# Kernel optimization log

Hardware: AMD Instinct MI355X
Metric: run time of the kernel (lower is better)

The kernel has to match this reference:

```python
import jax, jax.numpy as jnp
import numpy as np

B, NT, NP = 4096, 2048, 1024
DT = 1e-3


def _cum_trap(y, dx):
    # cumulative trapezoid along last dim, zero-prepended (preserve_dims=True)
    c = jnp.cumsum((y[..., 1:] + y[..., :-1]) * (0.5 * dx), axis=-1)
    return jnp.concatenate([jnp.zeros_like(y[..., :1]), c], axis=-1)


def _trapz(y, dx):
    return jnp.sum(y[..., :-1] + y[..., 1:], axis=-1) * (0.5 * dx)


def _renorm(f, dx):
    # square-normalize so each trace integrates to 1 (valid pdf)
    sq = f * f
    return sq / _trapz(sq, dx)[..., None]


def _natural_cubic_coeffs(p, q):
    # p: [NP] uniform knots, q: [B, NP] values -> per-interval coeffs a,b,c,d [B, NP-1]
    h = p[1] - p[0]
    n = p.shape[0]
    rhs = 6.0 * (q[..., :-2] - 2.0 * q[..., 1:-1] + q[..., 2:]) / (h * h)  # [B, n-2]
    m = n - 2
    A = 4.0 * jnp.eye(m, dtype=q.dtype) + jnp.eye(m, k=1, dtype=q.dtype) + jnp.eye(m, k=-1, dtype=q.dtype)
    M_int = jnp.linalg.solve(A, rhs.T).T                      # [B, n-2]
    zero = jnp.zeros_like(q[..., :1])
    M = jnp.concatenate([zero, M_int, zero], axis=-1)          # natural BC: M0 = Mn = 0
    a = q[..., :-1]
    b = (q[..., 1:] - q[..., :-1]) / h - h * (2.0 * M[..., :-1] + M[..., 1:]) / 6.0
    c = M[..., :-1] / 2.0
    d = (M[..., 1:] - M[..., :-1]) / (6.0 * h)
    return a, b, c, d


def _spline_eval(p, coeffs, x):
    # evaluate batched natural cubic splines at x: [B, NT]
    a, b, c, d = coeffs
    idx = jnp.clip(jnp.searchsorted(p, x, side='right') - 1, 0, p.shape[0] - 2)  # [B, NT]
    s = x - p[idx]
    ag = jnp.take_along_axis(a, idx, axis=-1)
    bg = jnp.take_along_axis(b, idx, axis=-1)
    cg = jnp.take_along_axis(c, idx, axis=-1)
    dg = jnp.take_along_axis(d, idx, axis=-1)
    return ag + s * (bg + s * (cg + s * dg))


def setup_inputs() -> dict:
    key = jax.random.key(0)
    k1, k2 = jax.random.split(key)
    f = jax.random.normal(k1, (B, NT), dtype=jnp.float32)
    obs_data = jax.random.normal(k2, (B, NT), dtype=jnp.float32)
    t = jnp.arange(NT, dtype=jnp.float32) * DT
    p = jnp.linspace(0.0, 1.0, NP, dtype=jnp.float32)
    return {"f": f, "obs_data": obs_data, "t": t, "p": p}


def reference(f, obs_data, t, p):
    dt = t[1] - t[0]
    # ---- __init__: build per-trace quantile splines from obs_data ----
    obs_tilde = _renorm(obs_data, dt)                 # [B, NT] pdf
    cdf_obs = _cum_trap(obs_tilde, dt)                # [B, NT] cdf
    # true_quantile: step lookup q(p) = t[searchsorted(cdf, p)]
    idx = jax.vmap(lambda c: jnp.searchsorted(c, p))(cdf_obs)
    idx = jnp.clip(idx, 0, t.shape[0] - 1)
    q = t[idx]                                        # [B, NP]
    coeffs = _natural_cubic_coeffs(p, q)
    # ---- forward: W2 distance ----
    f_tilde = _renorm(f, dt)                          # [B, NT]
    F = _cum_trap(f_tilde, dt)                        # [B, NT] cdf of f
    off_diag = _spline_eval(p, coeffs, F)             # Q_obs(F(t)) [B, NT]
    diff = (t[None, :] - off_diag) ** 2
    integrated = _trapz(diff * f_tilde, dt)           # [B]
    return integrated.sum()
```

## Files before the change

### kernel.cpp

```cpp
#include <hip/hip_runtime.h>

#define NBATCH 4096
#define NT 2048
#define NP 1024
#define NTH 256
#define EPT 8
#define MSZ 1022
#define KT 4
#define IMGW 14

__device__ __forceinline__ int pQ(int x) { return x + (x >> 3) + 9; }
__device__ __forceinline__ int pM(int x) { return x + (x >> 3); }

__global__ __launch_bounds__(NTH, 2) void w2loss_kernel(
    const float* __restrict__ f,
    const float* __restrict__ obs,
    float* __restrict__ partial)
{
    __shared__ float sQp[1168];
    __shared__ float sMp[1152];
    __shared__ float sH[NTH];
    __shared__ float sPow[IMGW];
    __shared__ float sWSA[4], sWSB[4];
    __shared__ float sSqA[2], sSqB[2];
    __shared__ float sRed[4];

    const int tid  = threadIdx.x;
    const int lane = tid & 63;
    const int wid  = tid >> 6;
    const int b    = blockIdx.x;
    const int base = tid * EPT;

    const float dt      = 0.001f;
    const float half_dt = 0.0005f;
    const float h       = 0.00097751710654936461f;
    const float inv_h   = 1023.0f;
    const float inv_h2  = 1046529.0f;
    const float h6      = h * (1.0f / 6.0f);
    const float ih6     = inv_h * (1.0f / 6.0f);

    const float* orow = obs + (size_t)b * NT;
    const float* frow = f   + (size_t)b * NT;
    float4 o0 = *reinterpret_cast<const float4*>(orow + base);
    float4 o1 = *reinterpret_cast<const float4*>(orow + base + 4);
    float4 g0 = *reinterpret_cast<const float4*>(frow + base);
    float4 g1 = *reinterpret_cast<const float4*>(frow + base + 4);

    if (tid < IMGW) {
        const float rho = -0.26794919243112270f;
        float v = 1.0f;
        for (int i = 0; i < tid; ++i) v *= rho;
        sPow[tid] = v;
    }

    float prefA[EPT], prefB[EPT];
    {
        float s0;
        s0 = o0.x*o0.x; prefA[0] = s0;
        s0 = o0.y*o0.y; prefA[1] = prefA[0] + s0;
        s0 = o0.z*o0.z; prefA[2] = prefA[1] + s0;
        s0 = o0.w*o0.w; prefA[3] = prefA[2] + s0;
        s0 = o1.x*o1.x; prefA[4] = prefA[3] + s0;
        s0 = o1.y*o1.y; prefA[5] = prefA[4] + s0;
        s0 = o1.z*o1.z; prefA[6] = prefA[5] + s0;
        s0 = o1.w*o1.w; prefA[7] = prefA[6] + s0;
        s0 = g0.x*g0.x; prefB[0] = s0;
        s0 = g0.y*g0.y; prefB[1] = prefB[0] + s0;
        s0 = g0.z*g0.z; prefB[2] = prefB[1] + s0;
        s0 = g0.w*g0.w; prefB[3] = prefB[2] + s0;
        s0 = g1.x*g1.x; prefB[4] = prefB[3] + s0;
        s0 = g1.y*g1.y; prefB[5] = prefB[4] + s0;
        s0 = g1.z*g1.z; prefB[6] = prefB[5] + s0;
        s0 = g1.w*g1.w; prefB[7] = prefB[6] + s0;
    }
    float sqA7 = o1.w * o1.w;
    float sqB7 = g1.w * g1.w;
    sH[tid] = sqA7;

    float tsA = prefA[EPT - 1], tsB = prefB[EPT - 1];
    float wsA = tsA, wsB = tsB;
#pragma unroll
    for (int off = 1; off < 64; off <<= 1) {
        float uA = __shfl_up(wsA, off);
        float uB = __shfl_up(wsB, off);
        if (lane >= off) { wsA += uA; wsB += uB; }
    }
    if (lane == 63) { sWSA[wid] = wsA; sWSB[wid] = wsB; }
    if (tid == 0)       { sSqA[0] = prefA[0]; sSqB[0] = prefB[0]; }
    if (tid == NTH - 1) { sSqA[1] = sqA7;     sSqB[1] = sqB7; }
    __syncthreads();

    float exclA = wsA - tsA, exclB = wsB - tsB;
    if (wid > 0) { exclA += sWSA[0]; exclB += sWSB[0]; }
    if (wid > 1) { exclA += sWSA[1]; exclB += sWSB[1]; }
    if (wid > 2) { exclA += sWSA[2]; exclB += sWSB[2]; }
    float totA = sWSA[0] + sWSA[1] + sWSA[2] + sWSA[3];
    float totB = sWSB[0] + sWSB[1] + sWSB[2] + sWSB[3];
    float sq0A = sSqA[0], sq0B = sSqB[0];
    float invSA = 1.0f / (half_dt * (2.0f * totA - sSqA[1] - sq0A));
    float invSB = 1.0f / (half_dt * (2.0f * totB - sSqB[1] - sq0B));

    {
        float cm;
        if (tid == 0) cm = -1.0f;
        else {
            float sqprev = sH[tid - 1];
            cm = half_dt * (((exclA - sqprev) + exclA) - sq0A) * invSA;
        }
        float Pm = exclA;
#pragma unroll
        for (int e = 0; e < EPT; ++e) {
            int j = base + e;
            float Pj = exclA + prefA[e];
            float cc = (j == 0) ? 0.0f : half_dt * (Pm + Pj - sq0A) * invSA;
            int kLo = (int)floorf(cm * inv_h) + 1;
            int kHi = (int)floorf(cc * inv_h);
            if (kLo < 0) kLo = 0;
            if (j == NT - 1) kHi = NP - 1;
            else {
                if (e == EPT - 1) kHi += 1;
                if (kHi > NP - 1) kHi = NP - 1;
            }
            float qv = (float)j * dt;
            for (int k = kLo; k <= kHi; ++k) sQp[pQ(k)] = qv;
            cm = cc;
            Pm = Pj;
        }
    }
    __syncthreads();

    {
        const float Cg = 0.28867513459481288f;
        const float CP[KT + 1] = {
            1.0f, -0.26794919243112270f, 0.071796769724490830f,
            -0.019237886466840586f, 0.0051547761428899979f };
        const int k0 = tid * 4;

        float qw[14];
#pragma unroll
        for (int x = 0; x < 14; ++x) qw[x] = sQp[pQ(k0 - 5 + x)];

        float r[12];
#pragma unroll
        for (int x = 0; x < 12; ++x) {
            int gi = k0 - 5 + x;
            float v = 6.0f * (qw[x] - 2.0f * qw[x + 1] + qw[x + 2]) * inv_h2;
            r[x] = (gi >= 0 && gi < MSZ) ? v : 0.0f;
        }

        float T1 = 0.0f, T2 = 0.0f;
        if (tid < 4) {
            float qe[15];
#pragma unroll
            for (int x = 0; x < 15; ++x) qe[x] = sQp[pQ(x)];
#pragma unroll
            for (int x = 0; x < IMGW - 1; ++x) {
                float rr = 6.0f * (qe[x] - 2.0f * qe[x + 1] + qe[x + 2]) * inv_h2;
                T1 += sPow[x + 1] * rr;
            }
        }
        if (tid >= NTH - 4) {
            float qe[15];
#pragma unroll
            for (int x = 0; x < 15; ++x) qe[x] = sQp[pQ(1009 + x)];
#pragma unroll
            for (int x = 0; x < IMGW - 1; ++x) {
                float rr = 6.0f * (qe[x] - 2.0f * qe[x + 1] + qe[x + 2]) * inv_h2;
                T2 += sPow[13 - x] * rr;
            }
        }

#pragma unroll
        for (int e = 0; e < 4; ++e) {
            int k = k0 + e;
            float acc = 0.0f;
#pragma unroll
            for (int d = -KT; d <= KT; ++d) {
                int ad = d < 0 ? -d : d;
                acc += CP[ad] * r[e + 4 + d];
            }
            if (k < IMGW)        acc -= sPow[k] * T1;
            if (1023 - k < IMGW) acc -= sPow[1023 - k] * T2;
            float mv = Cg * acc;
            if (k == 0 || k == NP - 1) mv = 0.0f;
            sMp[pM(k)] = mv;
        }
    }
    __syncthreads();

    float local = 0.0f;
    float term0 = 0.0f, term7 = 0.0f;
    {
        const float c1B = half_dt * invSB;
        const float K0  = (2.0f * exclB - sq0B) * c1B;
        float tj = (float)base * dt;
#pragma unroll
        for (int e = 0; e < EPT; ++e) {
            float Gj = (e ? prefB[e - 1] : 0.0f) + prefB[e];
            float Fj = __builtin_fmaf(Gj, c1B, K0);
            float sqe = e ? (prefB[e] - prefB[e - 1]) : prefB[0];
            float kf = Fj * inv_h;
            kf = fminf(fmaxf(kf, 0.0f), 1022.0f);
            int k = (int)kf;
            float s = __builtin_fmaf(-h, (float)k, Fj);
            float q0 = sQp[pQ(k)];
            float q1 = sQp[pQ(k + 1)];
            float M0 = sMp[pM(k)];
            float M1 = sMp[pM(k + 1)];
            float bco = (q1 - q0) * inv_h - (2.0f * M0 + M1) * h6;
            float od  = q0 + s * (bco + s * (0.5f * M0 + s * (M1 - M0) * ih6));
            float dd  = tj - od;
            float term = dd * dd * sqe;
            local += term;
            if (e == 0) term0 = term;
            if (e == EPT - 1) term7 = term;
            tj += dt;
        }
    }
    if (tid == 0)       local -= 0.5f * term0;
    if (tid == NTH - 1) local -= 0.5f * term7;

#pragma unroll
    for (int off = 32; off > 0; off >>= 1) local += __shfl_down(local, off);
    if (lane == 0) sRed[wid] = local;
    __syncthreads();
    if (tid == 0) partial[b] = (sRed[0] + sRed[1] + sRed[2] + sRed[3]) * (dt * invSB);
}

__global__ __launch_bounds__(NTH) void w2loss_reduce(
    const float* __restrict__ partial, float* __restrict__ out)
{
    __shared__ float sRed[4];
    const int tid  = threadIdx.x;
    const int lane = tid & 63;
    const int wid  = tid >> 6;
    float s = 0.0f;
#pragma unroll
    for (int i = 0; i < 16; i += 4) {
        float4 v = *reinterpret_cast<const float4*>(partial + tid * 16 + i);
        s += v.x + v.y + v.z + v.w;
    }
#pragma unroll
    for (int off = 32; off > 0; off >>= 1) s += __shfl_down(s, off);
    if (lane == 0) sRed[wid] = s;
    __syncthreads();
    if (tid == 0) out[0] = sRed[0] + sRed[1] + sRed[2] + sRed[3];
}

extern "C" void kernel_launch(void* const* d_in, const int* in_sizes, int n_in,
                              void* d_out, int out_size, void* d_ws, size_t ws_size,
                              hipStream_t stream) {
    const float* f   = (const float*)d_in[0];
    const float* obs = (const float*)d_in[1];
    float* out     = (float*)d_out;
    float* partial = (float*)d_ws;

    w2loss_kernel<<<NBATCH, NTH, 0, stream>>>(f, obs, partial);
    w2loss_reduce<<<1, NTH, 0, stream>>>(partial, out);
}
```

Measured before the change: 32.25 us.

## Process each batch row with a single wavefront instead of a 256-thread block

Each row is now handled by one 64-lane wavefront. Each lane covers 32 elements in four chunks, and the prefix sums use wave shuffles with a running carry, so the cross-wave shared-memory scans go away. The spline second-derivative solve gives each lane 16 knots, with the image-correction coefficients held as compile-time constants. Because a block is now a single wave, __syncthreads costs little and sync overhead drops. In exchange each thread carries much more register state and serial work, and there are only 4096 single-wave blocks to hide latency.

```diff
diff --git a/kernel.cpp b/kernel.cpp
--- a/kernel.cpp
+++ b/kernel.cpp
@@ -3,33 +3,21 @@
 #define NBATCH 4096
 #define NT 2048
 #define NP 1024
+#define KT 4
 #define NTH 256
-#define EPT 8
-#define MSZ 1022
-#define KT 4
-#define IMGW 14
-
-__device__ __forceinline__ int pQ(int x) { return x + (x >> 3) + 9; }
-__device__ __forceinline__ int pM(int x) { return x + (x >> 3); }
-
-__global__ __launch_bounds__(NTH, 2) void w2loss_kernel(
+
+__device__ __forceinline__ int pp(int x) { return x + (x >> 4); }
+
+__global__ __launch_bounds__(64, 4) void w2loss_kernel(
     const float* __restrict__ f,
     const float* __restrict__ obs,
     float* __restrict__ partial)
 {
-    __shared__ float sQp[1168];
-    __shared__ float sMp[1152];
-    __shared__ float sH[NTH];
-    __shared__ float sPow[IMGW];
-    __shared__ float sWSA[4], sWSB[4];
-    __shared__ float sSqA[2], sSqB[2];
-    __shared__ float sRed[4];
-
-    const int tid  = threadIdx.x;
-    const int lane = tid & 63;
-    const int wid  = tid >> 6;
+    __shared__ float sQp[1087];
+    __shared__ float sMp[1087];
+
+    const int lane = threadIdx.x;
     const int b    = blockIdx.x;
-    const int base = tid * EPT;
 
     const float dt      = 0.001f;
     const float half_dt = 0.0005f;
@@ -41,92 +29,118 @@
 
     const float* orow = obs + (size_t)b * NT;
     const float* frow = f   + (size_t)b * NT;
-    float4 o0 = *reinterpret_cast<const float4*>(orow + base);
-    float4 o1 = *reinterpret_cast<const float4*>(orow + base + 4);
-    float4 g0 = *reinterpret_cast<const float4*>(frow + base);
-    float4 g1 = *reinterpret_cast<const float4*>(frow + base + 4);
-
-    if (tid < IMGW) {
-        const float rho = -0.26794919243112270f;
-        float v = 1.0f;
-        for (int i = 0; i < tid; ++i) v *= rho;
-        sPow[tid] = v;
-    }
-
-    float prefA[EPT], prefB[EPT];
-    {
-        float s0;
-        s0 = o0.x*o0.x; prefA[0] = s0;
-        s0 = o0.y*o0.y; prefA[1] = prefA[0] + s0;
-        s0 = o0.z*o0.z; prefA[2] = prefA[1] + s0;
-        s0 = o0.w*o0.w; prefA[3] = prefA[2] + s0;
-        s0 = o1.x*o1.x; prefA[4] = prefA[3] + s0;
-        s0 = o1.y*o1.y; prefA[5] = prefA[4] + s0;
-        s0 = o1.z*o1.z; prefA[6] = prefA[5] + s0;
-        s0 = o1.w*o1.w; prefA[7] = prefA[6] + s0;
-        s0 = g0.x*g0.x; prefB[0] = s0;
-        s0 = g0.y*g0.y; prefB[1] = prefB[0] + s0;
-        s0 = g0.z*g0.z; prefB[2] = prefB[1] + s0;
-        s0 = g0.w*g0.w; prefB[3] = prefB[2] + s0;
-        s0 = g1.x*g1.x; prefB[4] = prefB[3] + s0;
-        s0 = g1.y*g1.y; prefB[5] = prefB[4] + s0;
-        s0 = g1.z*g1.z; prefB[6] = prefB[5] + s0;
-        s0 = g1.w*g1.w; prefB[7] = prefB[6] + s0;
-    }
-    float sqA7 = o1.w * o1.w;
-    float sqB7 = g1.w * g1.w;
-    sH[tid] = sqA7;
-
-    float tsA = prefA[EPT - 1], tsB = prefB[EPT - 1];
-    float wsA = tsA, wsB = tsB;
-#pragma unroll
-    for (int off = 1; off < 64; off <<= 1) {
-        float uA = __shfl_up(wsA, off);
-        float uB = __shfl_up(wsB, off);
-        if (lane >= off) { wsA += uA; wsB += uB; }
-    }
-    if (lane == 63) { sWSA[wid] = wsA; sWSB[wid] = wsB; }
-    if (tid == 0)       { sSqA[0] = prefA[0]; sSqB[0] = prefB[0]; }
-    if (tid == NTH - 1) { sSqA[1] = sqA7;     sSqB[1] = sqB7; }
-    __syncthreads();
-
-    float exclA = wsA - tsA, exclB = wsB - tsB;
-    if (wid > 0) { exclA += sWSA[0]; exclB += sWSB[0]; }
-    if (wid > 1) { exclA += sWSA[1]; exclB += sWSB[1]; }
-    if (wid > 2) { exclA += sWSA[2]; exclB += sWSB[2]; }
-    float totA = sWSA[0] + sWSA[1] + sWSA[2] + sWSA[3];
-    float totB = sWSB[0] + sWSB[1] + sWSB[2] + sWSB[3];
-    float sq0A = sSqA[0], sq0B = sSqB[0];
-    float invSA = 1.0f / (half_dt * (2.0f * totA - sSqA[1] - sq0A));
-    float invSB = 1.0f / (half_dt * (2.0f * totB - sSqB[1] - sq0B));
-
-    {
-        float cm;
-        if (tid == 0) cm = -1.0f;
-        else {
-            float sqprev = sH[tid - 1];
-            cm = half_dt * (((exclA - sqprev) + exclA) - sq0A) * invSA;
-        }
-        float Pm = exclA;
-#pragma unroll
-        for (int e = 0; e < EPT; ++e) {
-            int j = base + e;
-            float Pj = exclA + prefA[e];
-            float cc = (j == 0) ? 0.0f : half_dt * (Pm + Pj - sq0A) * invSA;
+
+    float4 ov[8], fv[8];
+#pragma unroll
+    for (int c = 0; c < 4; ++c) {
+        const int base = c * 512 + lane * 8;
+        ov[2*c]   = *reinterpret_cast<const float4*>(orow + base);
+        ov[2*c+1] = *reinterpret_cast<const float4*>(orow + base + 4);
+        fv[2*c]   = *reinterpret_cast<const float4*>(frow + base);
+        fv[2*c+1] = *reinterpret_cast<const float4*>(frow + base + 4);
+    }
+
+    float sq[32];
+    float excl[4], W6[4], W7[4], carry[4];
+    float run = 0.0f;
+#pragma unroll
+    for (int c = 0; c < 4; ++c) {
+        float4 a = ov[2*c], bb = ov[2*c+1];
+        sq[c*8+0]=a.x*a.x;  sq[c*8+1]=a.y*a.y;  sq[c*8+2]=a.z*a.z;  sq[c*8+3]=a.w*a.w;
+        sq[c*8+4]=bb.x*bb.x; sq[c*8+5]=bb.y*bb.y; sq[c*8+6]=bb.z*bb.z; sq[c*8+7]=bb.w*bb.w;
+        float p[8];
+        p[0] = sq[c*8];
+#pragma unroll
+        for (int e = 1; e < 8; ++e) p[e] = p[e-1] + sq[c*8+e];
+        float tsum = p[7];
+        float ws = tsum;
+#pragma unroll
+        for (int off = 1; off < 64; off <<= 1) {
+            float u = __shfl_up(ws, off);
+            if (lane >= off) ws += u;
+        }
+        float ex = ws - tsum;
+        excl[c] = ex;
+        float w6 = ex + p[6];
+        float w7 = ex + p[7];
+        W6[c] = __shfl(w6, 63);
+        W7[c] = __shfl(w7, 63);
+        carry[c] = run;
+        run = run + W7[c];
+    }
+    const float totA = run;
+    const float sq0A = __shfl(sq[0], 0);
+    const float sqLA = __shfl(sq[31], 63);
+    const float invSA = 1.0f / (half_dt * (2.0f * totA - sqLA - sq0A));
+
+#pragma unroll
+    for (int c = 0; c < 4; ++c) {
+        float p[8];
+        p[0] = sq[c*8];
+#pragma unroll
+        for (int e = 1; e < 8; ++e) p[e] = p[e-1] + sq[c*8+e];
+        float w6 = excl[c] + p[6];
+        float w7 = excl[c] + p[7];
+        float sw6 = __shfl_up(w6, 1);
+        float sw7 = __shfl_up(w7, 1);
+
+        float cm, Pm;
+        if (lane == 0) {
+            if (c == 0) { cm = -1.0f; Pm = 0.0f; }
+            else {
+                cm = half_dt * (((carry[c-1] + W6[c-1]) + (carry[c-1] + W7[c-1])) - sq0A) * invSA;
+                Pm = carry[c];
+            }
+        } else {
+            cm = half_dt * (((carry[c] + sw6) + (carry[c] + sw7)) - sq0A) * invSA;
+            Pm = carry[c] + sw7;
+        }
+
+#pragma unroll
+        for (int e = 0; e < 8; ++e) {
+            const int j = c * 512 + lane * 8 + e;
+            float Pj = carry[c] + (excl[c] + p[e]);
+            float cc = (j == 0) ? 0.0f : half_dt * ((Pm + Pj) - sq0A) * invSA;
             int kLo = (int)floorf(cm * inv_h) + 1;
-            int kHi = (int)floorf(cc * inv_h);
             if (kLo < 0) kLo = 0;
+            int kHi;
             if (j == NT - 1) kHi = NP - 1;
-            else {
-                if (e == EPT - 1) kHi += 1;
-                if (kHi > NP - 1) kHi = NP - 1;
-            }
-            float qv = (float)j * dt;
-            for (int k = kLo; k <= kHi; ++k) sQp[pQ(k)] = qv;
-            cm = cc;
-            Pm = Pj;
-        }
-    }
+            else { kHi = (int)floorf(cc * inv_h); if (kHi > NP - 1) kHi = NP - 1; }
+            const float qvj = (float)j * dt;
+            for (int k = kLo; k <= kHi; ++k) sQp[pp(k)] = qvj;
+            cm = cc; Pm = Pj;
+        }
+    }
+
+    float exB[4], W7B[4], carryB[4];
+    float runB = 0.0f;
+#pragma unroll
+    for (int c = 0; c < 4; ++c) {
+        float4 a = fv[2*c], bb = fv[2*c+1];
+        sq[c*8+0]=a.x*a.x;  sq[c*8+1]=a.y*a.y;  sq[c*8+2]=a.z*a.z;  sq[c*8+3]=a.w*a.w;
+        sq[c*8+4]=bb.x*bb.x; sq[c*8+5]=bb.y*bb.y; sq[c*8+6]=bb.z*bb.z; sq[c*8+7]=bb.w*bb.w;
+        float p[8];
+        p[0] = sq[c*8];
+#pragma unroll
+        for (int e = 1; e < 8; ++e) p[e] = p[e-1] + sq[c*8+e];
+        float tsum = p[7];
+        float ws = tsum;
+#pragma unroll
+        for (int off = 1; off < 64; off <<= 1) {
+            float u = __shfl_up(ws, off);
+            if (lane >= off) ws += u;
+        }
+        float ex = ws - tsum;
+        exB[c] = ex;
+        W7B[c] = __shfl(ex + p[7], 63);
+        carryB[c] = runB;
+        runB = runB + W7B[c];
+    }
+    const float totB = runB;
+    const float sq0B = __shfl(sq[0], 0);
+    const float sqLB = __shfl(sq[31], 63);
+    const float invSB = 1.0f / (half_dt * (2.0f * totB - sqLB - sq0B));
+
     __syncthreads();
 
     {
@@ -134,97 +148,103 @@
         const float CP[KT + 1] = {
             1.0f, -0.26794919243112270f, 0.071796769724490830f,
             -0.019237886466840586f, 0.0051547761428899979f };
-        const int k0 = tid * 4;
-
-        float qw[14];
-#pragma unroll
-        for (int x = 0; x < 14; ++x) qw[x] = sQp[pQ(k0 - 5 + x)];
-
-        float r[12];
-#pragma unroll
-        for (int x = 0; x < 12; ++x) {
-            int gi = k0 - 5 + x;
-            float v = 6.0f * (qw[x] - 2.0f * qw[x + 1] + qw[x + 2]) * inv_h2;
-            r[x] = (gi >= 0 && gi < MSZ) ? v : 0.0f;
-        }
-
-        float T1 = 0.0f, T2 = 0.0f;
-        if (tid < 4) {
-            float qe[15];
-#pragma unroll
-            for (int x = 0; x < 15; ++x) qe[x] = sQp[pQ(x)];
-#pragma unroll
-            for (int x = 0; x < IMGW - 1; ++x) {
-                float rr = 6.0f * (qe[x] - 2.0f * qe[x + 1] + qe[x + 2]) * inv_h2;
-                T1 += sPow[x + 1] * rr;
+        const float RPW[14] = {
+            1.0f, -0.26794919243112270f, 0.071796769724490830f,
+            -0.019237886466840586f, 0.0051547761428899979f,
+            -0.0013812184239975285f, 0.00037009627398250260f,
+            -9.9166998940445055e-05f, 2.6571322000000000e-05f,
+            -7.1197520000000000e-06f, 1.9076502000000000e-06f,
+            -5.1115295000000000e-07f, 1.3696300000000000e-07f,
+            -3.6699170000000000e-08f };
+
+        const int k0 = lane * 16;
+        float r[24];
+        {
+            int i0 = k0 - 5;
+            float q0r = sQp[pp(i0 < 0 ? 0 : i0)];
+            float q1r = sQp[pp(i0 + 1 < 0 ? 0 : i0 + 1)];
+#pragma unroll
+            for (int x = 0; x < 24; ++x) {
+                int gi = i0 + x;
+                int qi = gi + 2;
+                float q2r = sQp[pp(qi > 1023 ? 1023 : (qi < 0 ? 0 : qi))];
+                float v = 6.0f * (q0r - 2.0f * q1r + q2r) * inv_h2;
+                r[x] = (gi >= 0 && gi <= 1021) ? v : 0.0f;
+                q0r = q1r; q1r = q2r;
             }
         }
-        if (tid >= NTH - 4) {
-            float qe[15];
-#pragma unroll
-            for (int x = 0; x < 15; ++x) qe[x] = sQp[pQ(1009 + x)];
-#pragma unroll
-            for (int x = 0; x < IMGW - 1; ++x) {
-                float rr = 6.0f * (qe[x] - 2.0f * qe[x + 1] + qe[x + 2]) * inv_h2;
-                T2 += sPow[13 - x] * rr;
-            }
-        }
-
-#pragma unroll
-        for (int e = 0; e < 4; ++e) {
-            int k = k0 + e;
-            float acc = 0.0f;
-#pragma unroll
-            for (int d = -KT; d <= KT; ++d) {
-                int ad = d < 0 ? -d : d;
-                acc += CP[ad] * r[e + 4 + d];
-            }
-            if (k < IMGW)        acc -= sPow[k] * T1;
-            if (1023 - k < IMGW) acc -= sPow[1023 - k] * T2;
-            float mv = Cg * acc;
+
+        float acc[16];
+#pragma unroll
+        for (int m = 0; m < 16; ++m) {
+            float a = CP[0] * r[m + 4];
+#pragma unroll
+            for (int d = 1; d <= KT; ++d) a += CP[d] * (r[m + 4 - d] + r[m + 4 + d]);
+            acc[m] = a;
+        }
+        if (lane == 0) {
+            float T1 = 0.0f;
+#pragma unroll
+            for (int k2 = 0; k2 < 13; ++k2) T1 += RPW[k2 + 1] * r[5 + k2];
+#pragma unroll
+            for (int m = 1; m < 14; ++m) acc[m] -= RPW[m] * T1;
+        } else if (lane == 63) {
+            float T2 = 0.0f;
+#pragma unroll
+            for (int k2 = 0; k2 < 13; ++k2) T2 += RPW[13 - k2] * r[6 + k2];
+#pragma unroll
+            for (int m = 2; m < 15; ++m) acc[m] -= RPW[15 - m] * T2;
+        }
+#pragma unroll
+        for (int m = 0; m < 16; ++m) {
+            const int k = k0 + m;
+            float mv = Cg * acc[m];
             if (k == 0 || k == NP - 1) mv = 0.0f;
-            sMp[pM(k)] = mv;
-        }
-    }
+            sMp[pp(k)] = mv;
+        }
+    }
+
     __syncthreads();
 
-    float local = 0.0f;
-    float term0 = 0.0f, term7 = 0.0f;
-    {
-        const float c1B = half_dt * invSB;
-        const float K0  = (2.0f * exclB - sq0B) * c1B;
-        float tj = (float)base * dt;
-#pragma unroll
-        for (int e = 0; e < EPT; ++e) {
-            float Gj = (e ? prefB[e - 1] : 0.0f) + prefB[e];
-            float Fj = __builtin_fmaf(Gj, c1B, K0);
-            float sqe = e ? (prefB[e] - prefB[e - 1]) : prefB[0];
-            float kf = Fj * inv_h;
+    float local = 0.0f, term0 = 0.0f, term7 = 0.0f;
+    const float c1B = half_dt * invSB;
+#pragma unroll
+    for (int c = 0; c < 4; ++c) {
+        float p[8];
+        p[0] = sq[c*8];
+#pragma unroll
+        for (int e = 1; e < 8; ++e) p[e] = p[e-1] + sq[c*8+e];
+        const float bcc = carryB[c] + exB[c];
+#pragma unroll
+        for (int e = 0; e < 8; ++e) {
+            const int j = c * 512 + lane * 8 + e;
+            float sqe = sq[c*8+e];
+            float P = bcc + p[e];
+            float F = (((P - sqe) + P) - sq0B) * c1B;
+            float kf = F * inv_h;
             kf = fminf(fmaxf(kf, 0.0f), 1022.0f);
             int k = (int)kf;
-            float s = __builtin_fmaf(-h, (float)k, Fj);
-            float q0 = sQp[pQ(k)];
-            float q1 = sQp[pQ(k + 1)];
-            float M0 = sMp[pM(k)];
-            float M1 = sMp[pM(k + 1)];
+            float s = __builtin_fmaf(-h, (float)k, F);
+            float q0 = sQp[pp(k)];
+            float q1 = sQp[pp(k + 1)];
+            float M0 = sMp[pp(k)];
+            float M1 = sMp[pp(k + 1)];
             float bco = (q1 - q0) * inv_h - (2.0f * M0 + M1) * h6;
             float od  = q0 + s * (bco + s * (0.5f * M0 + s * (M1 - M0) * ih6));
+            float tj  = (float)j * dt;
             float dd  = tj - od;
             float term = dd * dd * sqe;
             local += term;
-            if (e == 0) term0 = term;
-            if (e == EPT - 1) term7 = term;
-            tj += dt;
-        }
-    }
-    if (tid == 0)       local -= 0.5f * term0;
-    if (tid == NTH - 1) local -= 0.5f * term7;
+            if (c == 0 && e == 0) term0 = term;
+            if (c == 3 && e == 7) term7 = term;
+        }
+    }
+    if (lane == 0)  local -= 0.5f * term0;
+    if (lane == 63) local -= 0.5f * term7;
 
 #pragma unroll
     for (int off = 32; off > 0; off >>= 1) local += __shfl_down(local, off);
-    if (lane == 0) sRed[wid] = local;
-    __syncthreads();
-    if (tid == 0) partial[b] = (sRed[0] + sRed[1] + sRed[2] + sRed[3]) * (dt * invSB);
+    if (lane == 0) partial[b] = local * (dt * invSB);
 }
 
 __global__ __launch_bounds__(NTH) void w2loss_reduce(
@@ -255,6 +275,6 @@
     float* out     = (float*)d_out;
     float* partial = (float*)d_ws;
 
-    w2loss_kernel<<<NBATCH, NTH, 0, stream>>>(f, obs, partial);
+    w2loss_kernel<<<NBATCH, 64, 0, stream>>>(f, obs, partial);
     w2loss_reduce<<<1, NTH, 0, stream>>>(partial, out);
 }
```

Result: slower. 52.67 us (+63.3%).
